# Kernel optimization log

Measured on AMD Instinct MI355X. Metric: run time of the kernel, lower is better.

## Reference

```python
import jax, jax.numpy as jnp
import numpy as np

# LightGCN propagation constants
N_USERS = 50000
N_ITEMS = 100000
N_NODES = N_USERS + N_ITEMS          # rows of the symmetric normalized adjacency
N_EDGES = 2400000                    # nnz of sparse adjacency (avg degree ~16)
LATENT_DIM = 64                      # config['latent_dim_rec']
N_LAYERS = 3                         # config['lightGCN_n_layers']
BATCH = 4096


def setup_inputs() -> dict:
    key = jax.random.key(0)
    ks = jax.random.split(key, 7)
    # Embedding tables, init std=0.1 as in nn.init.normal_(std=0.1)
    emb_user = 0.1 * jax.random.normal(ks[0], (N_USERS, LATENT_DIM), dtype=jnp.float32)
    emb_item = 0.1 * jax.random.normal(ks[1], (N_ITEMS, LATENT_DIM), dtype=jnp.float32)
    # Sparse normalized adjacency in COO form (fixed structure reused every layer)
    src = jax.random.randint(ks[2], (N_EDGES,), 0, N_NODES, dtype=jnp.int32)
    dst = jax.random.randint(ks[3], (N_EDGES,), 0, N_NODES, dtype=jnp.int32)
    # values ~ 1/sqrt(deg_i * deg_j) scale for avg degree 16
    vals = jax.random.uniform(ks[4], (N_EDGES,), dtype=jnp.float32) / 16.0
    users = jax.random.randint(ks[5], (BATCH,), 0, N_USERS, dtype=jnp.int32)
    items = jax.random.randint(ks[6], (BATCH,), 0, N_ITEMS, dtype=jnp.int32)
    return {"emb_user": emb_user, "emb_item": emb_item, "vals": vals,
            "src": src, "dst": dst, "users": users, "items": items}


def _spmm(vals, src, dst, x):
    # y[dst] += vals * x[src]  == torch.sparse.mm(G, x)
    return jax.ops.segment_sum(vals[:, None] * x[src], dst, num_segments=N_NODES)


def reference(emb_user, emb_item, vals, src, dst, users, items):
    # computer(): stack layer embeddings and mean-pool, fused as running sum
    all_emb = jnp.concatenate([emb_user, emb_item], axis=0)  # [N, D]
    acc = all_emb
    x = all_emb
    for _ in range(N_LAYERS):
        x = _spmm(vals, src, dst, x)
        acc = acc + x
    light_out = acc / jnp.asarray(N_LAYERS + 1, dtype=acc.dtype)
    users_emb = light_out[users]                 # [B, D]
    items_emb = light_out[N_USERS + items]       # [B, D]
    gamma = jnp.sum(users_emb * items_emb, axis=1)  # [B]
    return gamma
```

## Files before the change

### kernel.cpp

```cpp
#include <hip/hip_runtime.h>


#define N_USERS 50000
#define N_ITEMS 100000
#define N_NODES 150000
#define N_EDGES 2400000
#define DIM 64
#define BATCH 4096

#define CHUNKS 256
#define CHUNK_EDGES 9375
#define PPT 10
#define KB 256
#define NPB 586
#define ECAP 10240
#define GSTR 16
#define CONVB 2344

typedef unsigned int uint;
typedef float v2f __attribute__((ext_vector_type(2)));

__device__ __forceinline__ uint pack_bf16(float a, float b) {
    uint ua = __float_as_uint(a), ub = __float_as_uint(b);
    ua = (ua + 0x7FFFu + ((ua >> 16) & 1u)) >> 16;
    ub = (ub + 0x7FFFu + ((ub >> 16) & 1u)) >> 16;
    return ua | (ub << 16);
}

__device__ __forceinline__ v2f unpack_bf16x2(uint w) {
    v2f r;
    r.x = __uint_as_float(w << 16);
    r.y = __uint_as_float(w & 0xFFFF0000u);
    return r;
}

__global__ __launch_bounds__(1024) void part_kernel(
        const int* __restrict__ src, const int* __restrict__ dstA,
        const float* __restrict__ vals, int* __restrict__ gcur,
        int2* __restrict__ coarse,
        const float* __restrict__ emb_user, const float* __restrict__ emb_item,
        uint2* __restrict__ t0) {
    int t = threadIdx.x;
    if (blockIdx.x >= CHUNKS) {
        int i = (blockIdx.x - CHUNKS) * 1024 + t;
        if (i < N_NODES * DIM / 4) {
            const int userN4 = N_USERS * DIM / 4;
            float4 v;
            if (i < userN4) v = ((const float4*)emb_user)[i];
            else            v = ((const float4*)emb_item)[i - userN4];
            t0[i] = make_uint2(pack_bf16(v.x, v.y), pack_bf16(v.z, v.w));
        }
        return;
    }
    __shared__ int2 stage[CHUNK_EDGES];
    __shared__ unsigned char stage_b[CHUNK_EDGES];
    __shared__ int h[KB];
    __shared__ int hoff[KB];
    __shared__ int delta[KB];
    __shared__ int wsum4[4];
    int c = blockIdx.x;
    if (t < KB) h[t] = 0;
    __syncthreads();
    int base = c * CHUNK_EDGES;
    int d_c[PPT];
    int r_c[PPT];
#pragma unroll
    for (int u = 0; u < PPT; ++u) {
        int i = t + u * 1024;
        d_c[u] = 0;
        r_c[u] = 0;
        if (i < CHUNK_EDGES) {
            int d = dstA[base + i];
            d_c[u] = d;
            r_c[u] = atomicAdd(&h[(int)((unsigned)d / NPB)], 1);
        }
    }
    __syncthreads();
    int lane = t & 63, wid = t >> 6;
    if (t < KB) {
        int v = h[t];
        int incl = v;
#pragma unroll
        for (int o = 1; o < 64; o <<= 1) {
            int add = __shfl_up(incl, o, 64);
            if (lane >= o) incl += add;
        }
        hoff[t] = incl - v;
        if (lane == 63) wsum4[wid] = incl;
    }
    __syncthreads();
    if (t < 64) {
        int vv = (lane < 4) ? wsum4[lane] : 0;
        int inc2 = vv;
#pragma unroll
        for (int o = 1; o < 4; o <<= 1) {
            int add = __shfl_up(inc2, o, 64);
            if (lane >= o) inc2 += add;
        }
        if (lane < 4) wsum4[lane] = inc2 - vv;
    }
    __syncthreads();
    if (t < KB) {
        int off = hoff[t] + wsum4[t >> 6];
        hoff[t] = off;
        int cb = atomicAdd(&gcur[t * GSTR], h[t]);
        delta[t] = t * ECAP + cb - off;
    }
    __syncthreads();
#pragma unroll
    for (int u = 0; u < PPT; ++u) {
        int i = t + u * 1024;
        if (i < CHUNK_EDGES) {
            int e = base + i;
            int d = d_c[u];
            int b = (int)((unsigned)d / NPB);
            int dl = d - b * NPB;
            int pos = hoff[b] + r_c[u];
            stage[pos] = make_int2(src[e] | (dl << 18), __float_as_int(vals[e]));
            stage_b[pos] = (unsigned char)b;
        }
    }
    __syncthreads();
#pragma unroll
    for (int u = 0; u < PPT; ++u) {
        int j = t + u * 1024;
        if (j < CHUNK_EDGES) {
            int b = stage_b[j];
            int idx = j + delta[b];
            if (idx < (b + 1) * ECAP)
                coarse[idx] = stage[j];
        }
    }
}

__global__ __launch_bounds__(1024) void p4f_fine(int2* __restrict__ coarse,
                                                 const int* __restrict__ gcur,
                                                 uint* __restrict__ rowinfo) {
    __shared__ int2 eds[ECAP];
    __shared__ int cnt[640];
    __shared__ int rs_[640];
    __shared__ int cur_[640];
    __shared__ int wsum[16];
    int k = blockIdx.x, t = threadIdx.x;
    int rbase = k * ECAP;
    int ne = min(gcur[k * GSTR], ECAP);
    for (int i = t; i < ne; i += 1024) eds[i] = coarse[rbase + i];
    if (t < 640) cnt[t] = 0;
    __syncthreads();
    for (int i = t; i < ne; i += 1024)
        atomicAdd(&cnt[eds[i].x >> 18], 1);
    __syncthreads();
    int wid = t >> 6, lane = t & 63;
    if (t < 640) {
        int v = cnt[t];
        int incl = v;
#pragma unroll
        for (int o = 1; o < 64; o <<= 1) {
            int add = __shfl_up(incl, o, 64);
            if (lane >= o) incl += add;
        }
        rs_[t] = incl - v;
        if (lane == 63) wsum[wid] = incl;
    }
    __syncthreads();
    if (t < 64) {
        int vv = (lane < 10) ? wsum[lane] : 0;
        int inc2 = vv;
#pragma unroll
        for (int o = 1; o < 16; o <<= 1) {
            int add = __shfl_up(inc2, o, 64);
            if (lane >= o) inc2 += add;
        }
        if (lane < 10) wsum[lane] = inc2 - vv;
    }
    __syncthreads();
    if (t < 640) rs_[t] += wsum[wid];
    __syncthreads();
    int nodes0 = k * NPB;
    int nb = min(NPB, N_NODES - nodes0);
    if (t < nb)
        rowinfo[nodes0 + t] = (uint)(rbase + rs_[t]) | ((uint)cnt[t] << 22);
    if (t < 640) cur_[t] = rs_[t];
    __syncthreads();
    for (int i = t; i < ne; i += 1024) {
        int2 ev = eds[i];
        int dl = ev.x >> 18;
        int p = atomicAdd(&cur_[dl], 1);
        coarse[rbase + p] = make_int2(ev.x & 0x3FFFF, ev.y);
    }
}

__global__ __launch_bounds__(256) void spmm_kernel(
        const uint* __restrict__ rowinfo, const int2* __restrict__ epair,
        const uint* __restrict__ xin, uint* __restrict__ xout) {
    int wave = (blockIdx.x * 256 + threadIdx.x) >> 6;
    int lane = threadIdx.x & 63;
    int g = lane >> 3;
    int l = lane & 7;
    int n = wave * 8 + g;
    bool live = n < N_NODES;
    uint ri = live ? rowinfo[n] : 0u;
    int s = (int)(ri & 0x3FFFFFu);
    int e = live ? s + (int)(ri >> 22) : s;
    int gbase = g * 8;
    v2f a0 = {0.f, 0.f}, a1 = {0.f, 0.f}, a2 = {0.f, 0.f}, a3 = {0.f, 0.f};
    for (int jb = s; jb < e; jb += 8) {
        int jl = jb + l;
        int2 ev = epair[jl < e ? jl : (e - 1)];
        float vw = (jl < e) ? __int_as_float(ev.y) : 0.f;
        int sx = ev.x;
        int srcs[8];
        float ws[8];
#pragma unroll
        for (int u = 0; u < 8; ++u) {
            srcs[u] = __shfl(sx, gbase + u, 64);
            ws[u]   = __shfl(vw, gbase + u, 64);
        }
        uint4 r[8];
#pragma unroll
        for (int u = 0; u < 8; ++u)
            r[u] = ((const uint4*)(xin + (size_t)srcs[u] * 32))[l];
#pragma unroll
        for (int u = 0; u < 8; ++u) {
            a0 += ws[u] * unpack_bf16x2(r[u].x);
            a1 += ws[u] * unpack_bf16x2(r[u].y);
            a2 += ws[u] * unpack_bf16x2(r[u].z);
            a3 += ws[u] * unpack_bf16x2(r[u].w);
        }
    }
    if (live) {
        uint4 o;
        o.x = pack_bf16(a0.x, a0.y);
        o.y = pack_bf16(a1.x, a1.y);
        o.z = pack_bf16(a2.x, a2.y);
        o.w = pack_bf16(a3.x, a3.y);
        ((uint4*)(xout + (size_t)n * 32))[l] = o;
    }
}

__global__ __launch_bounds__(256) void batch_row_kernel(
        const int* __restrict__ users, const int* __restrict__ items,
        const float* __restrict__ emb_user, const float* __restrict__ emb_item,
        const uint* __restrict__ x1, const uint* __restrict__ x2,
        const uint* __restrict__ rowinfo, const int2* __restrict__ epair,
        float4* __restrict__ rows) {
    int w = (blockIdx.x * 256 + threadIdx.x) >> 6;
    int lane = threadIdx.x & 63;
    int g = lane >> 4;
    int l = lane & 15;
    bool isU = w < BATCH;
    int b = isU ? w : w - BATCH;
    int idx = isU ? users[b] : items[b];
    int n = isU ? idx : N_USERS + idx;
    uint ri = rowinfo[n];
    int s = (int)(ri & 0x3FFFFFu);
    int e = s + (int)(ri >> 22);
    v2f a0 = {0.f, 0.f}, a1 = {0.f, 0.f};
    for (int j0 = s + g; j0 < e; j0 += 16) {
        int2 ev[4];
        float vv[4];
        uint2 rr[4];
#pragma unroll
        for (int u = 0; u < 4; ++u) {
            int j = j0 + 4 * u;
            bool p = (u == 0) || (j < e);
            ev[u] = epair[p ? j : j0];
            vv[u] = p ? __int_as_float(ev[u].y) : 0.f;
        }
#pragma unroll
        for (int u = 0; u < 4; ++u)
            rr[u] = ((const uint2*)(x2 + (size_t)ev[u].x * 32))[l];
#pragma unroll
        for (int u = 0; u < 4; ++u) {
            a0 += vv[u] * unpack_bf16x2(rr[u].x);
            a1 += vv[u] * unpack_bf16x2(rr[u].y);
        }
    }
#pragma unroll
    for (int off = 16; off < 64; off <<= 1) {
        a0.x += __shfl_xor(a0.x, off, 64);
        a0.y += __shfl_xor(a0.y, off, 64);
        a1.x += __shfl_xor(a1.x, off, 64);
        a1.y += __shfl_xor(a1.y, off, 64);
    }
    if (g == 0) {
        const float* t0row = isU ? (emb_user + (size_t)idx * DIM)
                                 : (emb_item + (size_t)idx * DIM);
        float4 x0 = ((const float4*)t0row)[l];
        uint2 w1 = ((const uint2*)(x1 + (size_t)n * 32))[l];
        uint2 w2 = ((const uint2*)(x2 + (size_t)n * 32))[l];
        v2f b10 = unpack_bf16x2(w1.x), b11 = unpack_bf16x2(w1.y);
        v2f b20 = unpack_bf16x2(w2.x), b21 = unpack_bf16x2(w2.y);
        float4 r;
        r.x = x0.x + b10.x + b20.x + a0.x;
        r.y = x0.y + b10.y + b20.y + a0.y;
        r.z = x0.z + b11.x + b21.x + a1.x;
        r.w = x0.w + b11.y + b21.y + a1.y;
        rows[(size_t)w * 16 + l] = r;
    }
}

__global__ __launch_bounds__(256) void dot_kernel(const float* __restrict__ rows,
                                                  float* __restrict__ out) {
    int t = blockIdx.x * 256 + threadIdx.x;
    int b = t >> 6;
    int lane = t & 63;
    float p = rows[(size_t)b * DIM + lane] * rows[(size_t)(BATCH + b) * DIM + lane];
#pragma unroll
    for (int o = 32; o > 0; o >>= 1) p += __shfl_down(p, o, 64);
    if (lane == 0) out[b] = p * (1.0f / 16.0f);
}

extern "C" void kernel_launch(void* const* d_in, const int* in_sizes, int n_in,
                              void* d_out, int out_size, void* d_ws, size_t ws_size,
                              hipStream_t stream) {
    const float* emb_user = (const float*)d_in[0];
    const float* emb_item = (const float*)d_in[1];
    const float* vals     = (const float*)d_in[2];
    const int*   src      = (const int*)d_in[3];
    const int*   dst      = (const int*)d_in[4];
    const int*   users    = (const int*)d_in[5];
    const int*   items    = (const int*)d_in[6];
    float* out = (float*)d_out;

    char* ws = (char*)d_ws;
    size_t off = 0;
    auto walloc = [&](size_t bytes) -> void* {
        void* p = ws + off;
        off += (bytes + 255) & ~(size_t)255;
        return p;
    };
    const size_t ROWB = (size_t)N_NODES * DIM * 2;
    uint* t0          = (uint*)walloc(ROWB);
    uint* x1          = (uint*)walloc(ROWB);
    uint* x2          = (uint*)walloc(ROWB);
    int2* coarse      = (int2*)walloc((size_t)KB * ECAP * 8);
    int*  gcur        = (int*) walloc((size_t)KB * GSTR * 4);
    uint* rowinfo     = (uint*)walloc((size_t)N_NODES * 4);
    float4* rows      = (float4*)walloc((size_t)2 * BATCH * DIM * 4);

    hipMemsetAsync(gcur, 0, (size_t)KB * GSTR * 4, stream);

    part_kernel<<<CHUNKS + CONVB, 1024, 0, stream>>>(
        src, dst, vals, gcur, coarse, emb_user, emb_item, (uint2*)t0);
    p4f_fine<<<KB, 1024, 0, stream>>>(coarse, gcur, rowinfo);

    const int SPMM_BLOCKS = (N_NODES / 8 * 64 + 255) / 256;
    spmm_kernel<<<SPMM_BLOCKS, 256, 0, stream>>>(rowinfo, coarse, t0, x1);
    spmm_kernel<<<SPMM_BLOCKS, 256, 0, stream>>>(rowinfo, coarse, x1, x2);
    batch_row_kernel<<<(2 * BATCH) / 4, 256, 0, stream>>>(
        users, items, emb_user, emb_item, x1, x2, rowinfo, coarse, rows);
    dot_kernel<<<(BATCH * 64) / 256, 256, 0, stream>>>((const float*)rows, out);
}
```

Before: 244.0 us.

## Restrict second SpMM layer to rows reachable from batch nodes

Adds a mark kernel that flags every batch user/item node and its in-neighbors, then a compaction kernel that builds a list of active rows. The second propagation layer runs only over that list instead of all 150k rows, since the final layer is computed only for the batch rows. With 8192 batch nodes of average degree 16 the active set is a large fraction of all nodes, so the savings may be limited. It also adds two kernel launches and two memsets, and still launches the full grid.

```diff
diff --git a/kernel.cpp b/kernel.cpp
--- a/kernel.cpp
+++ b/kernel.cpp
@@ -190,6 +190,34 @@
     }
 }
 
+__global__ __launch_bounds__(256) void mark_kernel(
+        const int* __restrict__ users, const int* __restrict__ items,
+        const uint* __restrict__ rowinfo, const int2* __restrict__ epair,
+        unsigned char* __restrict__ flag) {
+    int w = (blockIdx.x * 256 + threadIdx.x) >> 6;
+    int lane = threadIdx.x & 63;
+    bool isU = w < BATCH;
+    int b = isU ? w : w - BATCH;
+    int idx = isU ? users[b] : items[b];
+    int n = isU ? idx : N_USERS + idx;
+    if (lane == 0) flag[n] = 1;
+    uint ri = rowinfo[n];
+    int s = (int)(ri & 0x3FFFFFu);
+    int e = s + (int)(ri >> 22);
+    for (int j = s + lane; j < e; j += 64)
+        flag[epair[j].x] = 1;
+}
+
+__global__ __launch_bounds__(256) void compact_kernel(
+        const unsigned char* __restrict__ flag, int* __restrict__ list,
+        int* __restrict__ gcount) {
+    int n = blockIdx.x * 256 + threadIdx.x;
+    if (n < N_NODES && flag[n]) {
+        int p = atomicAdd(gcount, 1);
+        list[p] = n;
+    }
+}
+
 __global__ __launch_bounds__(256) void spmm_kernel(
         const uint* __restrict__ rowinfo, const int2* __restrict__ epair,
         const uint* __restrict__ xin, uint* __restrict__ xout) {
@@ -199,6 +227,57 @@
     int l = lane & 7;
     int n = wave * 8 + g;
     bool live = n < N_NODES;
+    uint ri = live ? rowinfo[n] : 0u;
+    int s = (int)(ri & 0x3FFFFFu);
+    int e = live ? s + (int)(ri >> 22) : s;
+    int gbase = g * 8;
+    v2f a0 = {0.f, 0.f}, a1 = {0.f, 0.f}, a2 = {0.f, 0.f}, a3 = {0.f, 0.f};
+    for (int jb = s; jb < e; jb += 8) {
+        int jl = jb + l;
+        int2 ev = epair[jl < e ? jl : (e - 1)];
+        float vw = (jl < e) ? __int_as_float(ev.y) : 0.f;
+        int sx = ev.x;
+        int srcs[8];
+        float ws[8];
+#pragma unroll
+        for (int u = 0; u < 8; ++u) {
+            srcs[u] = __shfl(sx, gbase + u, 64);
+            ws[u]   = __shfl(vw, gbase + u, 64);
+        }
+        uint4 r[8];
+#pragma unroll
+        for (int u = 0; u < 8; ++u)
+            r[u] = ((const uint4*)(xin + (size_t)srcs[u] * 32))[l];
+#pragma unroll
+        for (int u = 0; u < 8; ++u) {
+            a0 += ws[u] * unpack_bf16x2(r[u].x);
+            a1 += ws[u] * unpack_bf16x2(r[u].y);
+            a2 += ws[u] * unpack_bf16x2(r[u].z);
+            a3 += ws[u] * unpack_bf16x2(r[u].w);
+        }
+    }
+    if (live) {
+        uint4 o;
+        o.x = pack_bf16(a0.x, a0.y);
+        o.y = pack_bf16(a1.x, a1.y);
+        o.z = pack_bf16(a2.x, a2.y);
+        o.w = pack_bf16(a3.x, a3.y);
+        ((uint4*)(xout + (size_t)n * 32))[l] = o;
+    }
+}
+
+__global__ __launch_bounds__(256) void spmm_list_kernel(
+        const uint* __restrict__ rowinfo, const int2* __restrict__ epair,
+        const uint* __restrict__ xin, uint* __restrict__ xout,
+        const int* __restrict__ list, const int* __restrict__ gcount) {
+    int wave = (blockIdx.x * 256 + threadIdx.x) >> 6;
+    int lane = threadIdx.x & 63;
+    int g = lane >> 3;
+    int l = lane & 7;
+    int i = wave * 8 + g;
+    int na = *gcount;
+    bool live = i < na;
+    int n = live ? list[i] : 0;
     uint ri = live ? rowinfo[n] : 0u;
     int s = (int)(ri & 0x3FFFFFu);
     int e = live ? s + (int)(ri >> 22) : s;
@@ -338,16 +417,27 @@
     int*  gcur        = (int*) walloc((size_t)KB * GSTR * 4);
     uint* rowinfo     = (uint*)walloc((size_t)N_NODES * 4);
     float4* rows      = (float4*)walloc((size_t)2 * BATCH * DIM * 4);
+    unsigned char* flag = (unsigned char*)walloc((size_t)N_NODES);
+    int* alist        = (int*)walloc((size_t)N_NODES * 4);
+    int* gcount       = (int*)walloc(256);
 
     hipMemsetAsync(gcur, 0, (size_t)KB * GSTR * 4, stream);
+    hipMemsetAsync(flag, 0, (size_t)N_NODES, stream);
+    hipMemsetAsync(gcount, 0, 4, stream);
 
     part_kernel<<<CHUNKS + CONVB, 1024, 0, stream>>>(
         src, dst, vals, gcur, coarse, emb_user, emb_item, (uint2*)t0);
     p4f_fine<<<KB, 1024, 0, stream>>>(coarse, gcur, rowinfo);
 
+    mark_kernel<<<(2 * BATCH) / 4, 256, 0, stream>>>(
+        users, items, rowinfo, coarse, flag);
+    compact_kernel<<<(N_NODES + 255) / 256, 256, 0, stream>>>(
+        flag, alist, gcount);
+
     const int SPMM_BLOCKS = (N_NODES / 8 * 64 + 255) / 256;
     spmm_kernel<<<SPMM_BLOCKS, 256, 0, stream>>>(rowinfo, coarse, t0, x1);
-    spmm_kernel<<<SPMM_BLOCKS, 256, 0, stream>>>(rowinfo, coarse, x1, x2);
+    spmm_list_kernel<<<SPMM_BLOCKS, 256, 0, stream>>>(
+        rowinfo, coarse, x1, x2, alist, gcount);
     batch_row_kernel<<<(2 * BATCH) / 4, 256, 0, stream>>>(
         users, items, emb_user, emb_item, x1, x2, rowinfo, coarse, rows);
     dot_kernel<<<(BATCH * 64) / 256, 256, 0, stream>>>((const float*)rows, out);
```

Result: slower. 267.0 us (+9.4%).
